# Kernel tuning notes

Hardware: AMD Instinct MI355X
Metric: run time of the kernel (lower is better)

Reference implementation:

```python
import jax, jax.numpy as jnp
import numpy as np

NUM_CLASSES = 80
TOPK = 9
EPS_OVERLAPS = 1e-6  # mmdet BboxOverlaps2D: union clamped to eps
EPS_YOLOV6 = 1e-9    # yolov6_iou_calculator: eps added to union


def _pairwise_iou(b1, b2, eps, add_eps):
    # b1: (..., M, 4), b2: (..., N, 4) xyxy -> (..., M, N)
    lt = jnp.maximum(b1[..., :, None, :2], b2[..., None, :, :2])
    rb = jnp.minimum(b1[..., :, None, 2:], b2[..., None, :, 2:])
    wh = jnp.clip(rb - lt, 0.0)
    overlap = wh[..., 0] * wh[..., 1]
    a1 = (b1[..., 2] - b1[..., 0]) * (b1[..., 3] - b1[..., 1])
    a2 = (b2[..., 2] - b2[..., 0]) * (b2[..., 3] - b2[..., 1])
    union = a1[..., :, None] + a2[..., None, :] - overlap
    return overlap / (union + eps) if add_eps else overlap / jnp.maximum(union, eps)


def _assign(pred_bboxes, priors, gt_labels, gt_bboxes, pad_bbox_flag, num_level_priors):
    num_level_priors = tuple(int(n) for n in np.asarray(num_level_priors))
    # priors (x, y, stride_w, stride_h) -> 5*stride cell boxes in xyxy
    cell_half = priors[:, 2:] * 2.5
    prior_boxes = jnp.concatenate([priors[:, :2] - cell_half, priors[:, :2] + cell_half], axis=-1)
    bs, num_gt = gt_bboxes.shape[0], gt_bboxes.shape[1]
    num_priors = priors.shape[0]
    gt_flat = gt_bboxes.reshape(-1, 4)

    # step 1: IoU between all priors and all gts
    overlaps = _pairwise_iou(gt_flat, prior_boxes, EPS_OVERLAPS, False).reshape(bs, num_gt, num_priors)

    # step 2: center distances
    gt_cxy = (gt_flat[:, :2] + gt_flat[:, 2:]) * 0.5
    prior_cxy = (prior_boxes[:, :2] + prior_boxes[:, 2:]) * 0.5
    dist = jnp.sqrt(jnp.sum((gt_cxy[:, None, :] - prior_cxy[None, :, :]) ** 2, axis=-1))
    dist = dist.reshape(bs, num_gt, num_priors)

    # step 3: per-level topk closest candidates
    pad_bool = pad_bbox_flag[..., 0] > 0  # (bs, num_gt)
    b_ix = jnp.arange(bs)[:, None, None]
    g_ix = jnp.arange(num_gt)[None, :, None]
    is_in_list, cand_list = [], []
    start = 0
    for pl in num_level_priors:
        k = min(TOPK, pl)
        d_l = jax.lax.dynamic_slice_in_dim(dist, start, pl, axis=-1)
        _, idx = jax.lax.top_k(-d_l, k)  # (bs, num_gt, k) smallest distances
        cand_list.append(idx + start)
        idx_m = jnp.where(pad_bool[..., None], idx, 0)
        counts = jnp.zeros((bs, num_gt, pl), dist.dtype).at[b_ix, g_ix, idx_m].add(1.0)
        is_in_list.append(jnp.where(counts > 1, jnp.zeros_like(counts), counts))
        start += pl
    is_in_candidate = jnp.concatenate(is_in_list, axis=-1)   # (bs, num_gt, num_priors)
    candidate_idxs = jnp.concatenate(cand_list, axis=-1)     # (bs, num_gt, k*levels)

    # step 4: mean + std of candidate IoUs as threshold
    candidate_overlaps = jnp.where(is_in_candidate > 0, overlaps, jnp.zeros_like(overlaps))
    gathered = jnp.take_along_axis(candidate_overlaps, candidate_idxs, axis=-1)
    thr = jnp.mean(gathered, axis=-1, keepdims=True) + jnp.std(gathered, axis=-1, keepdims=True, ddof=1)

    # step 5: keep candidates above threshold
    is_pos = jnp.where(candidate_overlaps > thr, is_in_candidate, jnp.zeros_like(is_in_candidate))

    # step 6: center of prior must lie inside gt box
    lt = prior_cxy[None, None, :, :] - gt_bboxes[:, :, None, :2]
    rb = gt_bboxes[:, :, None, 2:] - prior_cxy[None, None, :, :]
    is_in_gts = (jnp.minimum(lt, rb).min(axis=-1) > 1e-9).astype(gt_bboxes.dtype)

    pos_mask = is_pos * is_in_gts * pad_bbox_flag  # pad flag broadcasts (bs,num_gt,1)

    # resolve priors assigned to multiple gts: keep highest IoU gt
    fg = pos_mask.sum(axis=-2)  # (bs, num_priors)
    best_gt = jnp.argmax(overlaps, axis=1)  # (bs, num_priors)
    is_max = jax.nn.one_hot(best_gt, num_gt, dtype=pos_mask.dtype).transpose(0, 2, 1)
    pos_mask = jnp.where(fg[:, None, :] > 1, is_max, pos_mask)
    fg_mask = pos_mask.sum(axis=-2)                 # (bs, num_priors)
    gt_idx = jnp.argmax(pos_mask, axis=-2)          # (bs, num_priors)

    # targets
    flat_idx = gt_idx + jnp.arange(bs)[:, None] * num_gt
    assigned_labels = gt_labels.reshape(-1)[flat_idx]
    assigned_labels = jnp.where(fg_mask > 0, assigned_labels, NUM_CLASSES)
    assigned_bboxes = gt_bboxes.reshape(-1, 4)[flat_idx]
    assigned_scores = jax.nn.one_hot(assigned_labels, NUM_CLASSES + 1, dtype=gt_bboxes.dtype)[..., :NUM_CLASSES]

    # weight scores by IoU with predictions
    ious = _pairwise_iou(gt_bboxes, pred_bboxes, EPS_YOLOV6, True) * pos_mask
    assigned_scores = assigned_scores * jnp.max(ious, axis=-2)[..., None]
    return assigned_labels, assigned_bboxes, assigned_scores, fg_mask > 0


def setup_inputs() -> dict:
    key = jax.random.key(0)
    k0, k1, k2, k3, k4 = jax.random.split(key, 5)
    bs, num_gt, img = 32, 64, 640
    strides = (8, 16, 32)
    pri = []
    for s in strides:
        n = img // s
        xs = (np.arange(n, dtype=np.float32) + 0.5) * s
        gy, gx = np.meshgrid(xs, xs, indexing='ij')
        pts = np.stack([gx.ravel(), gy.ravel()], axis=1)
        st = np.full((pts.shape[0], 2), s, dtype=np.float32)
        pri.append(np.concatenate([pts, st], axis=1))
    priors = jnp.asarray(np.concatenate(pri, axis=0))  # (8400, 4)
    num_level_priors = (6400, 1600, 400)
    num_priors = priors.shape[0]
    cxy = jax.random.uniform(k0, (bs, num_gt, 2), minval=50.0, maxval=590.0)
    wh = jax.random.uniform(k1, (bs, num_gt, 2), minval=20.0, maxval=200.0)
    gt_bboxes = jnp.concatenate([cxy - wh * 0.5, cxy + wh * 0.5], axis=-1)
    gt_labels = jax.random.randint(k2, (bs, num_gt, 1), 0, NUM_CLASSES)
    pad_bbox_flag = jnp.ones((bs, num_gt, 1), jnp.float32)
    pcxy = priors[None, :, :2] + jax.random.normal(k3, (bs, num_priors, 2)) * 4.0
    pwh = jax.random.uniform(k4, (bs, num_priors, 2), minval=10.0, maxval=150.0)
    pred_bboxes = jnp.concatenate([pcxy - pwh * 0.5, pcxy + pwh * 0.5], axis=-1)
    return {'pred_bboxes': pred_bboxes, 'priors': priors, 'gt_labels': gt_labels,
            'gt_bboxes': gt_bboxes, 'pad_bbox_flag': pad_bbox_flag,
            'num_level_priors': num_level_priors}


def reference(pred_bboxes, priors, gt_labels, gt_bboxes, pad_bbox_flag, num_level_priors):
    return _assign(pred_bboxes, priors, gt_labels, gt_bboxes, pad_bbox_flag, num_level_priors)
```

## Files before the change

kernel.cpp:

```cpp
#include <hip/hip_runtime.h>

#define BS 32
#define NG 64
#define NP 8400
#define NTOPK 9
#define NUM_CLASSES 80
#define NCAND 27

__device__ __forceinline__ unsigned long long wave_min_u64_32(unsigned long long k) {
    #pragma unroll
    for (int off = 1; off < 32; off <<= 1) {
        unsigned long long o = __shfl_xor(k, off, 64);
        k = (o < k) ? o : k;
    }
    return k;
}

__global__ __launch_bounds__(256) void k_candidates(
    const float4* __restrict__ gt_bboxes,
    const float*  __restrict__ pad_flag,
    unsigned int* __restrict__ cand)
{
    const int bg   = (blockIdx.x * 256 + threadIdx.x) >> 6;
    const int lane = threadIdx.x & 63;

    const float4 gt  = gt_bboxes[bg];
    const float  pad = pad_flag[bg];
    const float  gcx = (gt.x + gt.z) * 0.5f;
    const float  gcy = (gt.y + gt.w) * 0.5f;
    const float  garea = (gt.z - gt.x) * (gt.w - gt.y);

    const float lvl_s[3] = {8.0f, 16.0f, 32.0f};
    const int   lvl_n[3] = {80, 40, 20};
    const int   lvl_b[3] = {0, 6400, 8000};

    float ov[NCAND];
    int   ixs[NCAND];
    float sum = 0.0f;

    const int dy5 = lane / 5;
    const int dx5 = lane - dy5 * 5;

    #pragma unroll
    for (int L = 0; L < 3; ++L) {
        const float s    = lvl_s[L];
        const int   n    = lvl_n[L];
        const int   base = lvl_b[L];

        int wx = (int)floorf(gcx / s) - 2;
        int wy = (int)floorf(gcy / s) - 2;
        wx = min(max(wx, 0), n - 5);
        wy = min(max(wy, 0), n - 5);

        unsigned long long key = ~0ull;
        if (lane < 25) {
            const int   iy  = wy + dy5;
            const int   ix  = wx + dx5;
            const float py  = ((float)iy + 0.5f) * s;
            const float px  = ((float)ix + 0.5f) * s;
            const float ddx = gcx - px;
            const float ddy = gcy - py;
            const float d   = sqrtf(ddx * ddx + ddy * ddy);
            key = ((unsigned long long)__float_as_uint(d) << 32) |
                  (unsigned int)(base + iy * n + ix);
        }

        const float hx = s * 2.5f;
        #pragma unroll
        for (int q = 0; q < NTOPK; ++q) {
            const unsigned long long m = wave_min_u64_32(key);
            if (key == m) key = ~0ull;

            const int slot = L * NTOPK + q;
            const int idx  = (int)(m & 0xffffffffu);
            const int rel  = idx - base;
            const int iy   = rel / n;
            const int ix   = rel - iy * n;
            const float px = ((float)ix + 0.5f) * s;
            const float py = ((float)iy + 0.5f) * s;
            const float px0 = px - hx, py0 = py - hx;
            const float px1 = px + hx, py1 = py + hx;
            float lx = fmaxf(gt.x, px0), ly = fmaxf(gt.y, py0);
            float rx = fminf(gt.z, px1), ry = fminf(gt.w, py1);
            float w = fmaxf(rx - lx, 0.0f), h = fmaxf(ry - ly, 0.0f);
            float ovl = w * h;
            float parea = (px1 - px0) * (py1 - py0);
            float o = ovl / fmaxf(garea + parea - ovl, 1e-6f);
            ov[slot]  = o;
            ixs[slot] = idx;
            sum += o;
        }
    }

    const float mean = sum / (float)NCAND;
    float var = 0.0f;
    #pragma unroll
    for (int i = 0; i < NCAND; ++i) {
        float d = ov[i] - mean;
        var += d * d;
    }
    const float thr = mean + sqrtf(var / (float)(NCAND - 1));

    unsigned int myval = 0xFFFFFFFFu;
    if (pad > 0.0f) {
        #pragma unroll
        for (int i = 0; i < NCAND; ++i) {
            bool pass = false;
            if (ov[i] > thr) {
                const int   L    = i / NTOPK;
                const float s    = lvl_s[L];
                const int   n    = lvl_n[L];
                const int   base = lvl_b[L];
                const int idx = ixs[i];
                const int rel = idx - base;
                const int iy  = rel / n;
                const int ix  = rel - iy * n;
                const float px = ((float)ix + 0.5f) * s;
                const float py = ((float)iy + 0.5f) * s;
                float mm = fminf(fminf(px - gt.x, py - gt.y),
                                 fminf(gt.z - px, gt.w - py));
                pass = (mm > 1e-9f);
            }
            if (lane == i && pass) myval = (unsigned int)ixs[i];
        }
    }
    if (lane < NCAND) cand[(size_t)bg * NCAND + lane] = myval;
}

__global__ __launch_bounds__(256) void k_write(
    const float4* __restrict__ priors,
    const float4* __restrict__ gt_bboxes,
    const int*    __restrict__ gt_labels,
    const float4* __restrict__ pred_bboxes,
    const unsigned int* __restrict__ cand,
    float* __restrict__ out)
{
    __shared__ float4 s_gt[NG];
    __shared__ int    s_lab[NG];
    __shared__ unsigned long long s_pos[256];
    __shared__ int    s_plab[256];
    __shared__ float  s_piou[256];

    const int b   = blockIdx.y;
    const int tid = threadIdx.x;
    const int p0  = blockIdx.x * 256;

    if (tid < NG) {
        s_gt[tid]  = gt_bboxes[b * NG + tid];
        s_lab[tid] = gt_labels[b * NG + tid];
    }
    s_pos[tid] = 0;
    __syncthreads();

    const unsigned int* bc = cand + (size_t)b * NG * NCAND;
    for (int e = tid; e < NG * NCAND; e += 256) {
        unsigned int idx = bc[e];
        unsigned int rel = idx - (unsigned int)p0;
        if (rel < 256u) {
            atomicOr(&s_pos[rel], 1ull << (e / NCAND));
        }
    }
    __syncthreads();

    const int p = p0 + tid;
    int   label  = NUM_CLASSES;
    float iou_w  = 0.0f;

    if (p < NP) {
        const size_t bp = (size_t)b * NP + p;
        unsigned long long mask = s_pos[tid];
        int fg = __popcll(mask);
        int gidx = 0;

        if (fg > 1) {
            float4 pr = priors[p];
            float hx = pr.z * 2.5f, hy = pr.w * 2.5f;
            float px0 = pr.x - hx, py0 = pr.y - hy, px1 = pr.x + hx, py1 = pr.y + hy;
            float parea = (px1 - px0) * (py1 - py0);
            float best = -1.0f;
            for (int gg = 0; gg < NG; ++gg) {
                float4 gtb = s_gt[gg];
                float lx = fmaxf(gtb.x, px0), ly = fmaxf(gtb.y, py0);
                float rx = fminf(gtb.z, px1), ry = fminf(gtb.w, py1);
                float w = fmaxf(rx - lx, 0.0f), h = fmaxf(ry - ly, 0.0f);
                float ovl = w * h;
                float ga = (gtb.z - gtb.x) * (gtb.w - gtb.y);
                float v = ovl / fmaxf(ga + parea - ovl, 1e-6f);
                if (v > best) { best = v; gidx = gg; }
            }
        } else if (fg == 1) {
            gidx = __ffsll((unsigned long long)mask) - 1;
        }

        const bool   fgm = fg > 0;
        const float4 gtb = s_gt[gidx];
        label = fgm ? s_lab[gidx] : NUM_CLASSES;

        if (fgm) {
            float4 pb = pred_bboxes[bp];
            float lx = fmaxf(gtb.x, pb.x), ly = fmaxf(gtb.y, pb.y);
            float rx = fminf(gtb.z, pb.z), ry = fminf(gtb.w, pb.w);
            float w = fmaxf(rx - lx, 0.0f), h = fmaxf(ry - ly, 0.0f);
            float ov = w * h;
            float ga = (gtb.z - gtb.x) * (gtb.w - gtb.y);
            float pa = (pb.z - pb.x) * (pb.w - pb.y);
            iou_w = ov / (ga + pa - ov + 1e-9f);
        }

        out[bp] = (float)label;
        ((float4*)(out + (size_t)BS * NP))[bp] = gtb;
        out[(size_t)BS * NP * 85 + bp] = fgm ? 1.0f : 0.0f;
    }

    s_plab[tid] = label;
    s_piou[tid] = iou_w;
    __syncthreads();

    const int npr  = min(256, NP - p0);
    const int nfl4 = npr * 20;
    float4* o4 = (float4*)(out + (size_t)BS * NP * 5 + ((size_t)b * NP + p0) * 80);
    for (int q = tid; q < nfl4; q += 256) {
        int pl   = q / 20;
        int comp = q - pl * 20;
        int lab  = s_plab[pl];
        float iw = s_piou[pl];
        int dd = lab - comp * 4;
        float4 v;
        v.x = (dd == 0) ? iw : 0.0f;
        v.y = (dd == 1) ? iw : 0.0f;
        v.z = (dd == 2) ? iw : 0.0f;
        v.w = (dd == 3) ? iw : 0.0f;
        o4[q] = v;
    }
}

extern "C" void kernel_launch(void* const* d_in, const int* in_sizes, int n_in,
                              void* d_out, int out_size, void* d_ws, size_t ws_size,
                              hipStream_t stream) {
    const float4* pred_bboxes = (const float4*)d_in[0];
    const float4* priors      = (const float4*)d_in[1];
    const int*    gt_labels   = (const int*)d_in[2];
    const float4* gt_bboxes   = (const float4*)d_in[3];
    const float*  pad_flag    = (const float*)d_in[4];

    unsigned int* cand = (unsigned int*)d_ws;

    k_candidates<<<dim3(BS * NG * 64 / 256), dim3(256), 0, stream>>>(
        gt_bboxes, pad_flag, cand);

    k_write<<<dim3((NP + 255) / 256, BS), dim3(256), 0, stream>>>(
        priors, gt_bboxes, gt_labels, pred_bboxes, cand, (float*)d_out);
}
```

Measured before the change: 125.1 us.

## Halve write tiles and prune candidate scatter by per-level window bounds

k_write now processes 128 priors per block instead of 256 with the same 256 threads, doubling the grid to 66x32 blocks. Rather than every block scanning all 1728 candidate entries for its batch, each thread handles one (gt, level) pair. It recomputes that pair's 5x5 window bounds and loads its 9 candidates only when the window overlaps the block's prior range. This is meant to cut redundant global reads and atomics in the scatter phase and add parallelism for the large output write. The cost is that half the threads sit idle in the per-prior phase and the gt/label preamble is duplicated across more blocks.

```diff
diff --git a/kernel.cpp b/kernel.cpp
--- a/kernel.cpp
+++ b/kernel.cpp
@@ -6,6 +6,9 @@
 #define NTOPK 9
 #define NUM_CLASSES 80
 #define NCAND 27
+
+#define TILE 128
+#define NTILE 66
 
 __device__ __forceinline__ unsigned long long wave_min_u64_32(unsigned long long k) {
     #pragma unroll
@@ -137,36 +140,52 @@
 {
     __shared__ float4 s_gt[NG];
     __shared__ int    s_lab[NG];
-    __shared__ unsigned long long s_pos[256];
-    __shared__ int    s_plab[256];
-    __shared__ float  s_piou[256];
+    __shared__ unsigned long long s_pos[TILE];
+    __shared__ int    s_plab[TILE];
+    __shared__ float  s_piou[TILE];
 
     const int b   = blockIdx.y;
     const int tid = threadIdx.x;
-    const int p0  = blockIdx.x * 256;
+    const int p0  = blockIdx.x * TILE;
+    const int npr = min(TILE, NP - p0);
 
     if (tid < NG) {
         s_gt[tid]  = gt_bboxes[b * NG + tid];
         s_lab[tid] = gt_labels[b * NG + tid];
     }
-    s_pos[tid] = 0;
+    if (tid < TILE) s_pos[tid] = 0;
     __syncthreads();
 
-    const unsigned int* bc = cand + (size_t)b * NG * NCAND;
-    for (int e = tid; e < NG * NCAND; e += 256) {
-        unsigned int idx = bc[e];
-        unsigned int rel = idx - (unsigned int)p0;
-        if (rel < 256u) {
-            atomicOr(&s_pos[rel], 1ull << (e / NCAND));
+    {
+        const int g    = tid >> 2;
+        const int part = tid & 3;
+        if (part < 3) {
+            const float s    = (part == 0) ? 8.0f : (part == 1) ? 16.0f : 32.0f;
+            const int   n    = (part == 0) ? 80   : (part == 1) ? 40    : 20;
+            const int   base = (part == 0) ? 0    : (part == 1) ? 6400  : 8000;
+            const float4 gt  = s_gt[g];
+            const float  gcx = (gt.x + gt.z) * 0.5f;
+            const float  gcy = (gt.y + gt.w) * 0.5f;
+            int wx = min(max((int)floorf(gcx / s) - 2, 0), n - 5);
+            int wy = min(max((int)floorf(gcy / s) - 2, 0), n - 5);
+            const int minidx = base + wy * n + wx;
+            const int maxidx = base + (wy + 4) * n + wx + 4;
+            if (maxidx >= p0 && minidx < p0 + npr) {
+                const unsigned int* e =
+                    cand + ((size_t)(b * NG + g)) * NCAND + part * NTOPK;
+                #pragma unroll
+                for (int k = 0; k < NTOPK; ++k) {
+                    unsigned int rel = e[k] - (unsigned int)p0;
+                    if (rel < (unsigned int)npr)
+                        atomicOr(&s_pos[rel], 1ull << g);
+                }
+            }
         }
     }
     __syncthreads();
 
-    const int p = p0 + tid;
-    int   label  = NUM_CLASSES;
-    float iou_w  = 0.0f;
-
-    if (p < NP) {
+    if (tid < npr) {
+        const int p = p0 + tid;
         const size_t bp = (size_t)b * NP + p;
         unsigned long long mask = s_pos[tid];
         int fg = __popcll(mask);
@@ -194,7 +213,8 @@
 
         const bool   fgm = fg > 0;
         const float4 gtb = s_gt[gidx];
-        label = fgm ? s_lab[gidx] : NUM_CLASSES;
+        const int  label = fgm ? s_lab[gidx] : NUM_CLASSES;
+        float iou_w = 0.0f;
 
         if (fgm) {
             float4 pb = pred_bboxes[bp];
@@ -210,13 +230,12 @@
         out[bp] = (float)label;
         ((float4*)(out + (size_t)BS * NP))[bp] = gtb;
         out[(size_t)BS * NP * 85 + bp] = fgm ? 1.0f : 0.0f;
-    }
-
-    s_plab[tid] = label;
-    s_piou[tid] = iou_w;
+
+        s_plab[tid] = label;
+        s_piou[tid] = iou_w;
+    }
     __syncthreads();
 
-    const int npr  = min(256, NP - p0);
     const int nfl4 = npr * 20;
     float4* o4 = (float4*)(out + (size_t)BS * NP * 5 + ((size_t)b * NP + p0) * 80);
     for (int q = tid; q < nfl4; q += 256) {
@@ -248,6 +267,6 @@
     k_candidates<<<dim3(BS * NG * 64 / 256), dim3(256), 0, stream>>>(
         gt_bboxes, pad_flag, cand);
 
-    k_write<<<dim3((NP + 255) / 256, BS), dim3(256), 0, stream>>>(
+    k_write<<<dim3(NTILE, BS), dim3(256), 0, stream>>>(
         priors, gt_bboxes, gt_labels, pred_bboxes, cand, (float*)d_out);
 }
```

Measured after the change: 130.9 us. 4.7% more time.
